# Kernel optimization log

Hardware: AMD Instinct MI355X
Metric: run time of the kernel (lower is better)

## Reference

```python
import jax, jax.numpy as jnp
import numpy as np

LN_EPS = 1e-5


def _ln(x, g, b):
    m = jnp.mean(x, axis=-1, keepdims=True)
    v = jnp.mean((x - m) ** 2, axis=-1, keepdims=True)
    return (x - m) * jax.lax.rsqrt(v + LN_EPS) * g + b


def _swish(x):
    return x * jax.nn.sigmoid(x)


def _ffn(x, w1, b1, w2, b2):
    return _swish(x @ w1 + b1) @ w2 + b2


def _dwconv(x, w, pad_l, pad_r):
    # x: (B,T,C), w: (C,K) depthwise kernel along time
    C = x.shape[-1]
    y = jax.lax.conv_general_dilated(
        jnp.transpose(x, (0, 2, 1)), w[:, None, :],
        window_strides=(1,), padding=[(pad_l, pad_r)],
        feature_group_count=C,
        dimension_numbers=('NCH', 'OIH', 'NCH'))
    return jnp.transpose(y, (0, 2, 1))


def _rel_shift(x):
    # NeMo Transformer-XL relative shift. x: (B,H,T,P)
    b, h, q, p = x.shape
    x = jnp.pad(x, ((0, 0), (0, 0), (0, 0), (1, 0)))
    x = x.reshape(b, h, p + 1, q)[:, :, 1:]
    return x.reshape(b, h, q, p)


def _mamba(x, in_proj_w, conv_w, conv_b, x_proj_w, dt_proj_w, dt_proj_b, A_log, D, out_proj_w):
    # Mamba1 selective-scan SSM. x: (B,T,d_model)
    B, T, _ = x.shape
    d_inner, d_state = A_log.shape
    dt_rank = dt_proj_w.shape[0]
    xi, z = jnp.split(x @ in_proj_w, 2, axis=-1)            # (B,T,d_inner) each
    K = conv_w.shape[1]
    xc = jax.nn.silu(_dwconv(xi, conv_w, K - 1, 0) + conv_b)  # causal depthwise conv
    dbc = xc @ x_proj_w
    dt = dbc[..., :dt_rank]
    Bs = dbc[..., dt_rank:dt_rank + d_state]                # (B,T,n)
    Cs = dbc[..., dt_rank + d_state:]                       # (B,T,n)
    dt = jax.nn.softplus(dt @ dt_proj_w + dt_proj_b)        # (B,T,d_inner)
    A = -jnp.exp(A_log)                                     # (d_inner,n)
    dA = jnp.exp(dt[..., None] * A)                         # (B,T,d,n)
    dBx = dt[..., None] * Bs[:, :, None, :] * xc[..., None]  # (B,T,d,n)

    def step(h, inp):
        dA_t, dBx_t, C_t = inp
        h = dA_t * h + dBx_t                                # (B,d,n)
        y = jnp.einsum('bdn,bn->bd', h, C_t)
        return h, y

    h0 = jnp.zeros((B, d_inner, d_state), x.dtype)
    _, ys = jax.lax.scan(step, h0, (jnp.moveaxis(dA, 1, 0), jnp.moveaxis(dBx, 1, 0), jnp.moveaxis(Cs, 1, 0)))
    y = jnp.moveaxis(ys, 0, 1) + D * xc
    y = y * jax.nn.silu(z)
    return y @ out_proj_w


def _rel_attn(x, pos_emb, wq, bq, wk, bk, wv, bv, w_pos, pbu, pbv, wo, bo):
    B, T, d = x.shape
    H = pbu.shape[0]
    dk = d // H
    q = (x @ wq + bq).reshape(B, T, H, dk)                  # (B,T,H,dk)
    k = (x @ wk + bk).reshape(B, T, H, dk).transpose(0, 2, 1, 3)
    v = (x @ wv + bv).reshape(B, T, H, dk).transpose(0, 2, 1, 3)
    p = (pos_emb @ w_pos).reshape(1, -1, H, dk).transpose(0, 2, 1, 3)  # (1,H,2T-1,dk)
    q_u = (q + pbu).transpose(0, 2, 1, 3)
    q_v = (q + pbv).transpose(0, 2, 1, 3)
    ac = jnp.einsum('bhqd,bhkd->bhqk', q_u, k)
    bd = jnp.einsum('bhqd,xhpd->bhqp', q_v, p)
    bd = _rel_shift(bd)[:, :, :, :T]
    scores = (ac + bd) / jnp.sqrt(jnp.asarray(dk, x.dtype))
    attn = jax.nn.softmax(scores, axis=-1)
    out = jnp.einsum('bhqk,bhkd->bhqd', attn, v).transpose(0, 2, 1, 3).reshape(B, T, d)
    return out @ wo + bo


def _conv_module(x, pw1_w, pw1_b, dw_w, dw_b, bn_g, bn_b, pw2_w, pw2_b):
    a = x @ pw1_w + pw1_b
    h, g = jnp.split(a, 2, axis=-1)
    y = h * jax.nn.sigmoid(g)                               # GLU
    K = dw_w.shape[1]
    y = _dwconv(y, dw_w, (K - 1) // 2, (K - 1) // 2) + dw_b
    # BatchNorm in eval mode with running stats (mean=0, var=1)
    y = y * jax.lax.rsqrt(jnp.asarray(1.0 + LN_EPS, x.dtype)) * bn_g + bn_b
    return _swish(y) @ pw2_w + pw2_b


def _forward(x, pos_emb,
             ln1_g, ln1_b, ff1_w1, ff1_b1, ff1_w2, ff1_b2,
             mamba_ln_g, mamba_ln_b, in_proj_w, mconv_w, mconv_b, x_proj_w,
             dt_proj_w, dt_proj_b, A_log, D, out_proj_w,
             mlp_ln_g, mlp_ln_b, mlp_fc1_w, mlp_fc1_b, mlp_fc2_w, mlp_fc2_b,
             att_ln_g, att_ln_b, wq, bq, wk, bk, wv, bv, w_pos, pos_bias_u, pos_bias_v, wo, bo,
             conv_ln_g, conv_ln_b, pw1_w, pw1_b, dw_w, dw_b, bn_g, bn_b, pw2_w, pw2_b,
             ln2_g, ln2_b, ff2_w1, ff2_b1, ff2_w2, ff2_b2,
             out_ln_g, out_ln_b):
    # FFN1 (half-step)
    r = x + 0.5 * _ffn(_ln(x, ln1_g, ln1_b), ff1_w1, ff1_b1, ff1_w2, ff1_b2)
    # Mamba SSM block (prenorm residual, fc_factor=1)
    r = r + _mamba(_ln(r, mamba_ln_g, mamba_ln_b), in_proj_w, mconv_w, mconv_b,
                   x_proj_w, dt_proj_w, dt_proj_b, A_log, D, out_proj_w)
    # Gated MLP sublayer of the SSM block
    h = _ln(r, mlp_ln_g, mlp_ln_b) @ mlp_fc1_w + mlp_fc1_b
    u, g = jnp.split(h, 2, axis=-1)
    r = r + (u * jax.nn.silu(g)) @ mlp_fc2_w + mlp_fc2_b
    # Rel-pos self attention
    r = r + _rel_attn(_ln(r, att_ln_g, att_ln_b), pos_emb, wq, bq, wk, bk, wv, bv,
                      w_pos, pos_bias_u, pos_bias_v, wo, bo)
    # Conformer conv module
    r = r + _conv_module(_ln(r, conv_ln_g, conv_ln_b), pw1_w, pw1_b, dw_w, dw_b,
                         bn_g, bn_b, pw2_w, pw2_b)
    # FFN2 (half-step)
    r = r + 0.5 * _ffn(_ln(r, ln2_g, ln2_b), ff2_w1, ff2_b1, ff2_w2, ff2_b2)
    return _ln(r, out_ln_g, out_ln_b)


def setup_inputs() -> dict:
    key = jax.random.key(0)
    B, T, d = 8, 1024, 512
    d_ff = 2048
    n_heads, dk = 8, 64
    expand, d_state, d_conv = 2, 16, 4
    d_inner = expand * d
    dt_rank = d // 16
    mlp_hidden = 2 * d
    K = 31
    ks = iter(jax.random.split(key, 40))

    def rn(shape, s=0.02):
        return jax.random.normal(next(ks), shape, jnp.float32) * s

    f32 = jnp.float32
    inp = dict(
        x=jax.random.normal(next(ks), (B, T, d), f32),
        pos_emb=jax.random.normal(next(ks), (1, 2 * T - 1, d), f32),
        ln1_g=jnp.ones((d,), f32), ln1_b=jnp.zeros((d,), f32),
        ff1_w1=rn((d, d_ff)), ff1_b1=jnp.zeros((d_ff,), f32),
        ff1_w2=rn((d_ff, d)), ff1_b2=jnp.zeros((d,), f32),
        mamba_ln_g=jnp.ones((d,), f32), mamba_ln_b=jnp.zeros((d,), f32),
        in_proj_w=rn((d, 2 * d_inner)),
        mconv_w=rn((d_inner, d_conv), 0.1), mconv_b=jnp.zeros((d_inner,), f32),
        x_proj_w=rn((d_inner, dt_rank + 2 * d_state)),
        dt_proj_w=rn((dt_rank, d_inner), 0.1),
        dt_proj_b=jnp.full((d_inner,), float(np.log(np.expm1(0.01))), f32),
        A_log=jnp.log(jnp.broadcast_to(jnp.arange(1, d_state + 1, dtype=f32), (d_inner, d_state)) + 0.0),
        D=jnp.ones((d_inner,), f32),
        out_proj_w=rn((d_inner, d)),
        mlp_ln_g=jnp.ones((d,), f32), mlp_ln_b=jnp.zeros((d,), f32),
        mlp_fc1_w=rn((d, 2 * mlp_hidden)), mlp_fc1_b=jnp.zeros((2 * mlp_hidden,), f32),
        mlp_fc2_w=rn((mlp_hidden, d)), mlp_fc2_b=jnp.zeros((d,), f32),
        att_ln_g=jnp.ones((d,), f32), att_ln_b=jnp.zeros((d,), f32),
        wq=rn((d, d)), bq=jnp.zeros((d,), f32),
        wk=rn((d, d)), bk=jnp.zeros((d,), f32),
        wv=rn((d, d)), bv=jnp.zeros((d,), f32),
        w_pos=rn((d, d)),
        pos_bias_u=rn((n_heads, dk)), pos_bias_v=rn((n_heads, dk)),
        wo=rn((d, d)), bo=jnp.zeros((d,), f32),
        conv_ln_g=jnp.ones((d,), f32), conv_ln_b=jnp.zeros((d,), f32),
        pw1_w=rn((d, 2 * d)), pw1_b=jnp.zeros((2 * d,), f32),
        dw_w=rn((d, K), 0.1), dw_b=jnp.zeros((d,), f32),
        bn_g=jnp.ones((d,), f32), bn_b=jnp.zeros((d,), f32),
        pw2_w=rn((d, d)), pw2_b=jnp.zeros((d,), f32),
        ln2_g=jnp.ones((d,), f32), ln2_b=jnp.zeros((d,), f32),
        ff2_w1=rn((d, d_ff)), ff2_b1=jnp.zeros((d_ff,), f32),
        ff2_w2=rn((d_ff, d)), ff2_b2=jnp.zeros((d,), f32),
        out_ln_g=jnp.ones((d,), f32), out_ln_b=jnp.zeros((d,), f32),
    )
    return inp


def reference(x, pos_emb,
              ln1_g, ln1_b, ff1_w1, ff1_b1, ff1_w2, ff1_b2,
              mamba_ln_g, mamba_ln_b, in_proj_w, mconv_w, mconv_b, x_proj_w,
              dt_proj_w, dt_proj_b, A_log, D, out_proj_w,
              mlp_ln_g, mlp_ln_b, mlp_fc1_w, mlp_fc1_b, mlp_fc2_w, mlp_fc2_b,
              att_ln_g, att_ln_b, wq, bq, wk, bk, wv, bv, w_pos, pos_bias_u, pos_bias_v, wo, bo,
              conv_ln_g, conv_ln_b, pw1_w, pw1_b, dw_w, dw_b, bn_g, bn_b, pw2_w, pw2_b,
              ln2_g, ln2_b, ff2_w1, ff2_b1, ff2_w2, ff2_b2,
              out_ln_g, out_ln_b):
    return _forward(x, pos_emb,
                    ln1_g, ln1_b, ff1_w1, ff1_b1, ff1_w2, ff1_b2,
                    mamba_ln_g, mamba_ln_b, in_proj_w, mconv_w, mconv_b, x_proj_w,
                    dt_proj_w, dt_proj_b, A_log, D, out_proj_w,
                    mlp_ln_g, mlp_ln_b, mlp_fc1_w, mlp_fc1_b, mlp_fc2_w, mlp_fc2_b,
                    att_ln_g, att_ln_b, wq, bq, wk, bk, wv, bv, w_pos, pos_bias_u, pos_bias_v, wo, bo,
                    conv_ln_g, conv_ln_b, pw1_w, pw1_b, dw_w, dw_b, bn_g, bn_b, pw2_w, pw2_b,
                    ln2_g, ln2_b, ff2_w1, ff2_b1, ff2_w2, ff2_b2,
                    out_ln_g, out_ln_b)
```

## Files before the change

### kernel.cpp

```cpp
#include <hip/hip_runtime.h>


typedef __bf16 bf16;
typedef __bf16 bf16x8 __attribute__((ext_vector_type(8)));
typedef __bf16 bf16x4 __attribute__((ext_vector_type(4)));
typedef float  f32x4  __attribute__((ext_vector_type(4)));

__device__ __forceinline__ float sigmf(float x) { return 1.f / (1.f + __expf(-x)); }
__device__ __forceinline__ float softplusf(float x) { return x > 20.f ? x : log1pf(__expf(x)); }

#define GL16(gsrc, ldst) \
  __builtin_amdgcn_global_load_lds((const __attribute__((address_space(1))) void*)(gsrc), \
                                   (__attribute__((address_space(3))) void*)(ldst), 16, 0, 0)

struct PrepEnt { const float* src; unsigned long long dstOff; int K, N, stride, mode, blk0, pad; };
#define NPREP 21
struct PrepTab { PrepEnt e[NPREP]; };

__global__ __launch_bounds__(256) void prep_weights(PrepTab tab, char* ws)
{
  int e = 0;
  for (int i = 1; i < NPREP; ++i) if ((int)blockIdx.x >= tab.e[i].blk0) e = i;
  PrepEnt en = tab.e[e];
  int lb = blockIdx.x - en.blk0;
  int tid = threadIdx.x;
  if (en.mode == 0) {
    __shared__ float t[32][33];
    int nTk = (en.K + 31) >> 5;
    int kt = lb % nTk, nt = lb / nTk;
    int k0 = kt * 32, n0 = nt * 32;
    int c = tid & 31, r0 = tid >> 5;
#pragma unroll
    for (int p = 0; p < 4; ++p) {
      int r = r0 + p * 8;
      int gk = k0 + r, gn = n0 + c;
      t[r][c] = (gk < en.K && gn < en.N) ? en.src[(size_t)gk * en.N + gn] : 0.f;
    }
    __syncthreads();
    bf16* dst = (bf16*)(ws + en.dstOff);
#pragma unroll
    for (int p = 0; p < 4; ++p) {
      int r = r0 + p * 8;
      int gn = n0 + r, gk = k0 + c;
      if (gn < en.N && gk < en.K) dst[(size_t)gn * en.stride + gk] = (bf16)t[c][r];
    }
  } else if (en.mode == 1) {
    size_t total = (size_t)en.K * en.N;
    size_t i0 = (size_t)lb * 2048 + (size_t)tid * 8;
    if (i0 < total) {
      bf16* dst = (bf16*)(ws + en.dstOff);
#pragma unroll
      for (int i = 0; i < 8; ++i) dst[i0 + i] = (bf16)en.src[i0 + i];
    }
  } else {
    int i0 = lb * 256 + tid;
    if (i0 < en.N) ((float*)(ws + en.dstOff))[i0] = en.src[i0];
  }
}

template<int MODE>
__global__ __launch_bounds__(256)
void gemm_k(const bf16* __restrict__ A, const bf16* __restrict__ W,
            const float* __restrict__ bias, const float* __restrict__ res,
            float* __restrict__ outF, bf16* __restrict__ outB,
            int M, int N, int K)
{
  __shared__ __align__(16) char As[128 * 128];
  __shared__ __align__(16) char Bs[128 * 128];
  const int tid = threadIdx.x;
  const int w = tid >> 6, l = tid & 63, l15 = l & 15, lg = l >> 4;
  const int wr = w >> 1, wc = w & 1;
  const int m0 = blockIdx.y * 128, n0 = blockIdx.x * 128;
  const int Mm1 = M - 1;
  f32x4 acc[4][4] = {};

  for (int k0 = 0; k0 < K; k0 += 64) {
#pragma unroll
    for (int i = 0; i < 4; ++i) {
      int row = w * 32 + i * 8 + (l >> 3);
      int ar = m0 + row; ar = ar > Mm1 ? Mm1 : ar;
      GL16(A + (size_t)ar * K + k0 + (l & 7) * 8, As + (w * 32 + i * 8) * 128);
      GL16(W + (size_t)(n0 + row) * K + k0 + (l & 7) * 8, Bs + (w * 32 + i * 8) * 128);
    }
    __syncthreads();
#pragma unroll
    for (int ks = 0; ks < 2; ++ks) {
      bf16x8 af[4], bfv[4];
#pragma unroll
      for (int mi = 0; mi < 4; ++mi)
        af[mi] = *(const bf16x8*)(As + (wr * 64 + mi * 16 + l15) * 128 + (ks * 4 + lg) * 16);
#pragma unroll
      for (int ni = 0; ni < 4; ++ni)
        bfv[ni] = *(const bf16x8*)(Bs + (wc * 64 + ni * 16 + l15) * 128 + (ks * 4 + lg) * 16);
#pragma unroll
      for (int mi = 0; mi < 4; ++mi)
#pragma unroll
        for (int ni = 0; ni < 4; ++ni)
          acc[mi][ni] = __builtin_amdgcn_mfma_f32_16x16x32_bf16(af[mi], bfv[ni], acc[mi][ni], 0, 0, 0);
    }
    __syncthreads();
  }

#pragma unroll
  for (int ni = 0; ni < 4; ++ni) {
    int col = n0 + wc * 64 + ni * 16 + l15;
    float bvl = 0.f;
    if constexpr (MODE == 2 || MODE == 3 || MODE == 4 || MODE == 5 || MODE == 7) bvl = bias[col];
#pragma unroll
    for (int mi = 0; mi < 4; ++mi) {
#pragma unroll
      for (int r = 0; r < 4; ++r) {
        int row = m0 + wr * 64 + mi * 16 + lg * 4 + r;
        if (row >= M) continue;
        float v = acc[mi][ni][r];
        size_t oi = (size_t)row * N + col;
        if constexpr (MODE == 0) { outF[oi] = v; }
        else if constexpr (MODE == 1) { outB[oi] = (bf16)v; }
        else if constexpr (MODE == 2) { outB[oi] = (bf16)(v + bvl); }
        else if constexpr (MODE == 3) { float t = v + bvl; outB[oi] = (bf16)(t * sigmf(t)); }
        else if constexpr (MODE == 4) { outF[oi] = res[oi] + v + bvl; }
        else if constexpr (MODE == 5) { outF[oi] = res[oi] + 0.5f * (v + bvl); }
        else if constexpr (MODE == 6) { outF[oi] = res[oi] + v; }
        else if constexpr (MODE == 7) { outF[oi] = softplusf(v + bvl); }
        else if constexpr (MODE == 8) {
          int hd = col >> 6;
          outB[((size_t)hd * 2047 + row) * 64 + (col & 63)] = (bf16)v;
        }
      }
    }
  }
}

template<bool F32OUT>
__global__ __launch_bounds__(128)
void ln_k(const float* __restrict__ in, const float* __restrict__ g,
          const float* __restrict__ bb, void* __restrict__ out)
{
  int row = blockIdx.x, t = threadIdx.x;
  float4 v = ((const float4*)(in + (size_t)row * 512))[t];
  float s  = v.x + v.y + v.z + v.w;
  float s2 = v.x * v.x + v.y * v.y + v.z * v.z + v.w * v.w;
#pragma unroll
  for (int o = 1; o < 64; o <<= 1) { s += __shfl_xor(s, o); s2 += __shfl_xor(s2, o); }
  __shared__ float sh[4];
  if ((t & 63) == 0) { sh[(t >> 6) * 2] = s; sh[(t >> 6) * 2 + 1] = s2; }
  __syncthreads();
  s = sh[0] + sh[2]; s2 = sh[1] + sh[3];
  float mean = s * (1.f / 512.f);
  float var  = s2 * (1.f / 512.f) - mean * mean;
  float rstd = rsqrtf(var + 1e-5f);
  float4 gg = ((const float4*)g)[t], bv = ((const float4*)bb)[t];
  float o0 = (v.x - mean) * rstd * gg.x + bv.x;
  float o1 = (v.y - mean) * rstd * gg.y + bv.y;
  float o2 = (v.z - mean) * rstd * gg.z + bv.z;
  float o3 = (v.w - mean) * rstd * gg.w + bv.w;
  if constexpr (F32OUT) {
    ((float4*)out)[(size_t)row * 128 + t] = make_float4(o0, o1, o2, o3);
  } else {
    bf16x4 ob; ob[0] = (bf16)o0; ob[1] = (bf16)o1; ob[2] = (bf16)o2; ob[3] = (bf16)o3;
    ((bf16x4*)out)[(size_t)row * 128 + t] = ob;
  }
}

template<int VAR>
__global__ __launch_bounds__(256)
void glu_k(const bf16* __restrict__ in, void* __restrict__ out,
           int halfN, int fullN, int shift)
{
  int gid = blockIdx.x * 256 + threadIdx.x;
  int m = gid >> shift;
  int j = (gid & ((1 << shift) - 1)) * 8;
  bf16x8 uv = *(const bf16x8*)(in + (size_t)m * fullN + j);
  bf16x8 gv = *(const bf16x8*)(in + (size_t)m * fullN + halfN + j);
  if constexpr (VAR == 0) {
    bf16x8 o;
#pragma unroll
    for (int i = 0; i < 8; ++i) {
      float gf = (float)gv[i];
      o[i] = (bf16)((float)uv[i] * gf * sigmf(gf));
    }
    *(bf16x8*)((bf16*)out + (size_t)m * halfN + j) = o;
  } else {
    float* of = (float*)out + (size_t)m * halfN + j;
    float4 a, b;
    a.x = (float)uv[0] * sigmf((float)gv[0]); a.y = (float)uv[1] * sigmf((float)gv[1]);
    a.z = (float)uv[2] * sigmf((float)gv[2]); a.w = (float)uv[3] * sigmf((float)gv[3]);
    b.x = (float)uv[4] * sigmf((float)gv[4]); b.y = (float)uv[5] * sigmf((float)gv[5]);
    b.z = (float)uv[6] * sigmf((float)gv[6]); b.w = (float)uv[7] * sigmf((float)gv[7]);
    *(float4*)of = a; *(float4*)(of + 4) = b;
  }
}

__global__ __launch_bounds__(256)
void extract_dt(const float* __restrict__ dbc, bf16* __restrict__ dtb)
{
  int gid = blockIdx.x * 256 + threadIdx.x;
  int m = gid >> 3, j = (gid & 7) * 8;
  bf16x8 o;
#pragma unroll
  for (int i = 0; i < 8; ++i) {
    int c = j + i;
    o[i] = (bf16)(c < 32 ? dbc[(size_t)m * 128 + c] : 0.f);
  }
  *(bf16x8*)(dtb + (size_t)m * 64 + j) = o;
}

__global__ __launch_bounds__(256)
void dwconv4_k(const bf16* __restrict__ xz, const float* __restrict__ cw,
               const float* __restrict__ cb, bf16* __restrict__ xcb)
{
  const int c  = blockIdx.x * 256 + threadIdx.x;
  const int t0 = blockIdx.y * 16;
  const int b  = blockIdx.z;
  const bf16* xb = xz + (size_t)b * 1024 * 2048 + c;
  float win[19];
#pragma unroll
  for (int j = 0; j < 19; ++j) {
    int tt = t0 - 3 + j;
    win[j] = (tt >= 0) ? (float)xb[(size_t)tt * 2048] : 0.f;
  }
  float w0 = cw[c * 4], w1 = cw[c * 4 + 1], w2 = cw[c * 4 + 2], w3 = cw[c * 4 + 3];
  float cbv = cb[c];
  bf16* ob = xcb + (size_t)(b * 1024 + t0) * 1024 + c;
#pragma unroll
  for (int i = 0; i < 16; ++i) {
    float acc = cbv + win[i] * w0 + win[i + 1] * w1 + win[i + 2] * w2 + win[i + 3] * w3;
    ob[(size_t)i * 1024] = (bf16)(acc * sigmf(acc));
  }
}

__global__ __launch_bounds__(256)
void dwconv31_k(const float* __restrict__ y, const float* __restrict__ dw,
                const float* __restrict__ db, const float* __restrict__ bg,
                const float* __restrict__ bb, bf16* __restrict__ outb)
{
  const int c  = blockIdx.x * 256 + threadIdx.x;
  const int t0 = blockIdx.y * 32;
  const int b  = blockIdx.z;
  const float* yb = y + (size_t)b * 1024 * 512 + c;
  float win[62];
#pragma unroll
  for (int j = 0; j < 62; ++j) {
    int tt = t0 - 15 + j;
    win[j] = (tt >= 0 && tt < 1024) ? yb[(size_t)tt * 512] : 0.f;
  }
  float wt[31];
#pragma unroll
  for (int k = 0; k < 31; ++k) wt[k] = dw[c * 31 + k];
  const float bgv = bg[c] * rsqrtf(1.f + 1e-5f);
  const float bbv = bb[c], dbv = db[c];
  bf16* ob = outb + (size_t)(b * 1024 + t0) * 512 + c;
#pragma unroll
  for (int i = 0; i < 32; ++i) {
    float acc = dbv;
#pragma unroll
    for (int k = 0; k < 31; ++k) acc += win[i + k] * wt[k];
    float v = acc * bgv + bbv;
    ob[(size_t)i * 512] = (bf16)(v * sigmf(v));
  }
}

__global__ __launch_bounds__(128)
void scan_k(const float* __restrict__ dt, const bf16* __restrict__ xc,
            const bf16* __restrict__ xz, const float* __restrict__ dbc,
            const float* __restrict__ alog, const float* __restrict__ Dp,
            bf16* __restrict__ ym)
{
  __shared__ __align__(16) float dtb[2][64][32];
  __shared__ __align__(16) bf16  xcb[2][64][32];
  __shared__ __align__(16) bf16  zbb[2][64][32];
  __shared__ __align__(16) float bcb[2][64][32];
  __shared__ __align__(16) float yp[64][128];
  __shared__ float Ds[32];

  const int tid = threadIdx.x;
  const int w = tid >> 6, l = tid & 63;
  const int ch = tid >> 2;
  const int s  = tid & 3;
  const int b  = blockIdx.x >> 5, dc = blockIdx.x & 31;
  const int d0 = dc * 32;
  const int d  = d0 + ch;

  const float A0 = -__expf(alog[d * 16 + s * 4 + 0]);
  const float A1 = -__expf(alog[d * 16 + s * 4 + 1]);
  const float A2 = -__expf(alog[d * 16 + s * 4 + 2]);
  const float A3 = -__expf(alog[d * 16 + s * 4 + 3]);
  if (tid < 32) Ds[tid] = Dp[d0 + tid];
  float h0 = 0.f, h1 = 0.f, h2 = 0.f, h3 = 0.f;
  const size_t rb = (size_t)b * 1024;

  auto stage = [&](int bu, int c) {
    size_t t0 = rb + (size_t)c * 64;
#pragma unroll
    for (int i = 0; i < 4; ++i) {
      int r = w * 32 + i * 8 + (l >> 3);
      GL16(dt + (t0 + r) * 1024 + d0 + (l & 7) * 4, &dtb[bu][w * 32 + i * 8][0]);
    }
#pragma unroll
    for (int i = 0; i < 4; ++i) {
      int r = w * 32 + i * 8 + (l >> 3);
      GL16(dbc + (t0 + r) * 128 + 32 + (l & 7) * 4, &bcb[bu][w * 32 + i * 8][0]);
    }
#pragma unroll
    for (int i = 0; i < 2; ++i) {
      int r = w * 32 + i * 16 + (l >> 2);
      GL16(xc + (t0 + r) * 1024 + d0 + (l & 3) * 8, &xcb[bu][w * 32 + i * 16][0]);
      GL16(xz + (t0 + r) * 2048 + 1024 + d0 + (l & 3) * 8, &zbb[bu][w * 32 + i * 16][0]);
    }
  };

  stage(0, 0);
  __syncthreads();
  int bu = 0;
  for (int c = 0; c < 16; ++c) {
    if (c < 15) stage(bu ^ 1, c + 1);
#pragma unroll 8
    for (int t = 0; t < 64; ++t) {
      float dtv = dtb[bu][t][ch];
      float xcv = (float)xcb[bu][t][ch];
      float4 Bv = *(const float4*)&bcb[bu][t][s * 4];
      float4 Cv = *(const float4*)&bcb[bu][t][16 + s * 4];
      float dtx = dtv * xcv;
      h0 = __expf(dtv * A0) * h0 + dtx * Bv.x;
      h1 = __expf(dtv * A1) * h1 + dtx * Bv.y;
      h2 = __expf(dtv * A2) * h2 + dtx * Bv.z;
      h3 = __expf(dtv * A3) * h3 + dtx * Bv.w;
      yp[t][tid] = h0 * Cv.x + h1 * Cv.y + h2 * Cv.z + h3 * Cv.w;
    }
    __syncthreads();
    {
      size_t t0 = rb + (size_t)c * 64;
#pragma unroll
      for (int j = 0; j < 16; ++j) {
        int idx = j * 128 + tid;
        int t = idx >> 5, cc = idx & 31;
        float4 p = *(const float4*)&yp[t][cc * 4];
        float xcv = (float)xcb[bu][t][cc];
        float zv  = (float)zbb[bu][t][cc];
        float o = (p.x + p.y + p.z + p.w + Ds[cc] * xcv) * (zv * sigmf(zv));
        ym[(t0 + t) * 1024 + d0 + cc] = (bf16)o;
      }
    }
    __syncthreads();
    bu ^= 1;
  }
}

__global__ __launch_bounds__(256)
void attnprep_k(const bf16* __restrict__ qkv, const float* __restrict__ pbu,
                const float* __restrict__ pbv, bf16* __restrict__ qu,
                bf16* __restrict__ qv, bf16* __restrict__ kb)
{
  int gid = blockIdx.x * 256 + threadIdx.x;
  int dd = (gid & 7) * 8;
  int t  = (gid >> 3) & 1023;
  int h  = (gid >> 13) & 7;
  int b  = gid >> 16;
  size_t src = ((size_t)(b * 1024 + t)) * 1536 + h * 64 + dd;
  bf16x8 q = *(const bf16x8*)(qkv + src);
  bf16x8 k = *(const bf16x8*)(qkv + src + 512);
  size_t dst = (((size_t)(b * 8 + h)) * 1024 + t) * 64 + dd;
  bf16x8 ou, ov;
#pragma unroll
  for (int i = 0; i < 8; ++i) {
    float qf = (float)q[i];
    ou[i] = (bf16)(qf + pbu[h * 64 + dd + i]);
    ov[i] = (bf16)(qf + pbv[h * 64 + dd + i]);
  }
  *(bf16x8*)(qu + dst) = ou;
  *(bf16x8*)(qv + dst) = ov;
  *(bf16x8*)(kb + dst) = k;
}

__global__ __launch_bounds__(256)
void vtrans_k(const bf16* __restrict__ qkv, bf16* __restrict__ vt)
{
  __shared__ __align__(16) bf16 tile[64][80];
  int tid = threadIdx.x;
  int t0 = blockIdx.x * 64, h = blockIdx.y, b = blockIdx.z;
#pragma unroll
  for (int j = 0; j < 2; ++j) {
    int idx = tid + j * 256;
    int r = idx >> 3, c8 = (idx & 7) * 8;
    bf16x8 v = *(const bf16x8*)(qkv + ((size_t)(b * 1024 + t0 + r)) * 1536 + 1024 + h * 64 + c8);
    *(bf16x8*)(&tile[r][c8]) = v;
  }
  __syncthreads();
  size_t obase = ((size_t)(b * 8 + h)) * 64;
#pragma unroll
  for (int j = 0; j < 2; ++j) {
    int idx = tid + j * 256;
    int ddr = idx >> 3, tc = (idx & 7) * 8;
    bf16x8 o;
#pragma unroll
    for (int i = 0; i < 8; ++i) o[i] = tile[tc + i][ddr];
    *(bf16x8*)(vt + (obase + ddr) * 1024 + t0 + tc) = o;
  }
}

__global__ __launch_bounds__(256)
void attn_k(const bf16* __restrict__ qu, const bf16* __restrict__ qv,
            const bf16* __restrict__ kb, const bf16* __restrict__ vt,
            const bf16* __restrict__ ph, bf16* __restrict__ outb)
{
  __shared__ __align__(16) char Ks[64 * 128];
  __shared__ __align__(16) char Vs[64 * 128];
  __shared__ __align__(16) bf16 Pl[4][16][88];
  int tid = threadIdx.x, w = tid >> 6, l = tid & 63;
  int l15 = l & 15, lg = l >> 4;
  int qt = blockIdx.x, h = blockIdx.y, b = blockIdx.z;
  int bh = b * 8 + h;
  int qw0 = qt * 64 + w * 16;
  const bf16* kbh = kb + (size_t)bh * 65536;
  const bf16* vth = vt + (size_t)bh * 65536;
  const bf16* phh = ph + (size_t)h * 2047 * 64;

  bf16x8 aqu[2], aqv[2], onesf;
#pragma unroll
  for (int i = 0; i < 8; ++i) onesf[i] = (bf16)1.f;
  {
    size_t qb = ((size_t)bh * 1024 + qw0 + l15) * 64 + lg * 8;
    aqu[0] = *(const bf16x8*)(qu + qb);
    aqu[1] = *(const bf16x8*)(qu + qb + 32);
    aqv[0] = *(const bf16x8*)(qv + qb);
    aqv[1] = *(const bf16x8*)(qv + qb + 32);
  }
  f32x4 acco[4] = {};
  f32x4 accl = {};

  for (int kv = 0; kv < 16; ++kv) {
    int k0 = kv * 64;
#pragma unroll
    for (int j = 0; j < 2; ++j) {
      int idx = tid + j * 256;
      int row = idx >> 3, sl = idx & 7, ssl = sl ^ (row & 7);
      *(bf16x8*)(Ks + row * 128 + ssl * 16) = *(const bf16x8*)(kbh + (size_t)(k0 + row) * 64 + sl * 8);
      *(bf16x8*)(Vs + row * 128 + ssl * 16) = *(const bf16x8*)(vth + (size_t)row * 1024 + k0 + sl * 8);
    }
    __syncthreads();
    f32x4 sfr[4] = {};
    f32x4 efr[5] = {};
#pragma unroll
    for (int ni = 0; ni < 4; ++ni)
#pragma unroll
      for (int kt = 0; kt < 2; ++kt) {
        int row = ni * 16 + l15;
        int ssl = (kt * 4 + lg) ^ (row & 7);
        bf16x8 bv = *(const bf16x8*)(Ks + row * 128 + ssl * 16);
        sfr[ni] = __builtin_amdgcn_mfma_f32_16x16x32_bf16(aqu[kt], bv, sfr[ni], 0, 0, 0);
      }
    int rho0 = k0 - qw0 + 1008;
#pragma unroll
    for (int f = 0; f < 5; ++f) {
      int rho = rho0 + f * 16 + l15; if (rho > 2046) rho = 2046;
      const bf16* pp = phh + (size_t)rho * 64;
#pragma unroll
      for (int kt = 0; kt < 2; ++kt) {
        bf16x8 bv = *(const bf16x8*)(pp + kt * 32 + lg * 8);
        efr[f] = __builtin_amdgcn_mfma_f32_16x16x32_bf16(aqv[kt], bv, efr[f], 0, 0, 0);
      }
    }
#pragma unroll
    for (int r = 0; r < 4; ++r) {
      int qr = lg * 4 + r;
#pragma unroll
      for (int ni = 0; ni < 4; ++ni) {
        int j = ni * 16 + l15 - qr + 15;
        int srcl = (l & 48) | (j & 15);
        float v1 = __shfl(efr[ni][r], srcl, 64);
        float v2 = __shfl(efr[ni + 1][r], srcl, 64);
        float bd = ((j >> 4) == ni) ? v1 : v2;
        Pl[w][qr][ni * 16 + l15] = (bf16)__expf((sfr[ni][r] + bd) * 0.125f);
      }
    }
#pragma unroll
    for (int kt = 0; kt < 2; ++kt) {
      bf16x8 af = *(const bf16x8*)(&Pl[w][l15][kt * 32 + lg * 8]);
      accl = __builtin_amdgcn_mfma_f32_16x16x32_bf16(af, onesf, accl, 0, 0, 0);
#pragma unroll
      for (int ni = 0; ni < 4; ++ni) {
        int row = ni * 16 + l15;
        int ssl = (kt * 4 + lg) ^ (row & 7);
        bf16x8 bv = *(const bf16x8*)(Vs + row * 128 + ssl * 16);
        acco[ni] = __builtin_amdgcn_mfma_f32_16x16x32_bf16(af, bv, acco[ni], 0, 0, 0);
      }
    }
    __syncthreads();
  }
#pragma unroll
  for (int r = 0; r < 4; ++r) {
    float inv = 1.f / accl[r];
    int grow = b * 1024 + qw0 + lg * 4 + r;
#pragma unroll
    for (int ni = 0; ni < 4; ++ni)
      outb[(size_t)grow * 512 + h * 64 + ni * 16 + l15] = (bf16)(acco[ni][r] * inv);
  }
}

extern "C" void kernel_launch(void* const* d_in, const int* in_sizes, int n_in,
                              void* d_out, int out_size, void* d_ws, size_t ws_size,
                              hipStream_t stream)
{
  char* ws = (char*)d_ws;
  const float* x        = (const float*)d_in[0];
  const float* pos_emb  = (const float*)d_in[1];
  const float* ln1_g    = (const float*)d_in[2];
  const float* ln1_b    = (const float*)d_in[3];
  const float* ff1_w1   = (const float*)d_in[4];
  const float* ff1_b1   = (const float*)d_in[5];
  const float* ff1_w2   = (const float*)d_in[6];
  const float* ff1_b2   = (const float*)d_in[7];
  const float* mamba_ln_g = (const float*)d_in[8];
  const float* mamba_ln_b = (const float*)d_in[9];
  const float* in_proj_w  = (const float*)d_in[10];
  const float* mconv_w    = (const float*)d_in[11];
  const float* mconv_b    = (const float*)d_in[12];
  const float* x_proj_w   = (const float*)d_in[13];
  const float* dt_proj_w  = (const float*)d_in[14];
  const float* dt_proj_b  = (const float*)d_in[15];
  const float* A_log      = (const float*)d_in[16];
  const float* Dvec       = (const float*)d_in[17];
  const float* out_proj_w = (const float*)d_in[18];
  const float* mlp_ln_g   = (const float*)d_in[19];
  const float* mlp_ln_b   = (const float*)d_in[20];
  const float* mlp_fc1_w  = (const float*)d_in[21];
  const float* mlp_fc1_b  = (const float*)d_in[22];
  const float* mlp_fc2_w  = (const float*)d_in[23];
  const float* mlp_fc2_b  = (const float*)d_in[24];
  const float* att_ln_g   = (const float*)d_in[25];
  const float* att_ln_b   = (const float*)d_in[26];
  const float* wq  = (const float*)d_in[27];
  const float* bq  = (const float*)d_in[28];
  const float* wk  = (const float*)d_in[29];
  const float* bk  = (const float*)d_in[30];
  const float* wv  = (const float*)d_in[31];
  const float* bvv = (const float*)d_in[32];
  const float* w_pos = (const float*)d_in[33];
  const float* pbu   = (const float*)d_in[34];
  const float* pbv   = (const float*)d_in[35];
  const float* wo  = (const float*)d_in[36];
  const float* bo  = (const float*)d_in[37];
  const float* conv_ln_g = (const float*)d_in[38];
  const float* conv_ln_b = (const float*)d_in[39];
  const float* pw1_w = (const float*)d_in[40];
  const float* pw1_b = (const float*)d_in[41];
  const float* dw_w  = (const float*)d_in[42];
  const float* dw_b  = (const float*)d_in[43];
  const float* bn_g  = (const float*)d_in[44];
  const float* bn_b  = (const float*)d_in[45];
  const float* pw2_w = (const float*)d_in[46];
  const float* pw2_b = (const float*)d_in[47];
  const float* ln2_g = (const float*)d_in[48];
  const float* ln2_b = (const float*)d_in[49];
  const float* ff2_w1 = (const float*)d_in[50];
  const float* ff2_b1 = (const float*)d_in[51];
  const float* ff2_w2 = (const float*)d_in[52];
  const float* ff2_b2 = (const float*)d_in[53];
  const float* out_ln_g = (const float*)d_in[54];
  const float* out_ln_b = (const float*)d_in[55];

  size_t off = 0;
  auto alloc = [&](size_t bytes) { size_t r = off; off += (bytes + 255) & ~(size_t)255; return r; };
  const size_t o_ff1w1t  = alloc((size_t)2048 * 512 * 2);
  const size_t o_ff1w2t  = alloc((size_t)512 * 2048 * 2);
  const size_t o_inprojt = alloc((size_t)2048 * 512 * 2);
  const size_t o_xprojt  = alloc((size_t)128 * 1024 * 2);
  const size_t o_dtprojt = alloc((size_t)1024 * 64 * 2);
  const size_t o_outprojt= alloc((size_t)512 * 1024 * 2);
  const size_t o_fc1t    = alloc((size_t)2048 * 512 * 2);
  const size_t o_fc2t    = alloc((size_t)512 * 1024 * 2);
  const size_t o_wqkvt   = alloc((size_t)1536 * 512 * 2);
  const size_t o_wpost   = alloc((size_t)512 * 512 * 2);
  const size_t o_wot     = alloc((size_t)512 * 512 * 2);
  const size_t o_pw1t    = alloc((size_t)1024 * 512 * 2);
  const size_t o_pw2t    = alloc((size_t)512 * 512 * 2);
  const size_t o_ff2w1t  = alloc((size_t)2048 * 512 * 2);
  const size_t o_ff2w2t  = alloc((size_t)512 * 2048 * 2);
  const size_t o_posbf   = alloc((size_t)2047 * 512 * 2);
  const size_t o_pheads  = alloc((size_t)8 * 2047 * 64 * 2);
  const size_t o_bqkv    = alloc((size_t)1536 * 4);
  const size_t o_R       = alloc((size_t)8192 * 512 * 4);
  const size_t o_ABUF    = alloc((size_t)8192 * 512 * 2);
  const size_t o_GBUF    = alloc((size_t)8192 * 1024 * 2);
  const size_t o_DBC     = alloc((size_t)8192 * 128 * 4);
  const size_t o_DTBF    = alloc((size_t)8192 * 64 * 2);
  const size_t o_ARENA   = alloc((size_t)64 << 20);

  if (off > ws_size) return;

  bf16* ff1w1t  = (bf16*)(ws + o_ff1w1t);
  bf16* ff1w2t  = (bf16*)(ws + o_ff1w2t);
  bf16* inprojt = (bf16*)(ws + o_inprojt);
  bf16* xprojt  = (bf16*)(ws + o_xprojt);
  bf16* dtprojt = (bf16*)(ws + o_dtprojt);
  bf16* outprojt= (bf16*)(ws + o_outprojt);
  bf16* fc1t    = (bf16*)(ws + o_fc1t);
  bf16* fc2t    = (bf16*)(ws + o_fc2t);
  bf16* wqkvt   = (bf16*)(ws + o_wqkvt);
  bf16* wpost   = (bf16*)(ws + o_wpost);
  bf16* wot     = (bf16*)(ws + o_wot);
  bf16* pw1t    = (bf16*)(ws + o_pw1t);
  bf16* pw2t    = (bf16*)(ws + o_pw2t);
  bf16* ff2w1t  = (bf16*)(ws + o_ff2w1t);
  bf16* ff2w2t  = (bf16*)(ws + o_ff2w2t);
  bf16* posbf   = (bf16*)(ws + o_posbf);
  bf16* pheads  = (bf16*)(ws + o_pheads);
  float* bqkv   = (float*)(ws + o_bqkv);
  float* R      = (float*)(ws + o_R);
  bf16* ABUF    = (bf16*)(ws + o_ABUF);
  bf16* GBUF    = (bf16*)(ws + o_GBUF);
  float* GBUFf  = (float*)(ws + o_GBUF);
  float* DBC    = (float*)(ws + o_DBC);
  bf16* DTBF    = (bf16*)(ws + o_DTBF);
  char* ARENA   = ws + o_ARENA;
  bf16* BIGBF   = (bf16*)ARENA;
  bf16* XZB     = (bf16*)ARENA;
  float* DTF    = (float*)(ARENA + ((size_t)32 << 20));
  bf16* QKV     = (bf16*)ARENA;
  bf16* QU      = (bf16*)(ARENA + ((size_t)32 << 20));
  bf16* QV      = (bf16*)(ARENA + ((size_t)40 << 20));
  bf16* KB      = (bf16*)(ARENA + ((size_t)48 << 20));
  bf16* VT      = (bf16*)(ARENA + ((size_t)56 << 20));
  bf16* CBUF    = (bf16*)ARENA;
  float* OUT = (float*)d_out;

  (void)hipMemsetAsync(ws + o_xprojt, 0, (size_t)128 * 1024 * 2, stream);
  (void)hipMemsetAsync(ws + o_dtprojt, 0, (size_t)1024 * 64 * 2, stream);

  PrepTab tab;
  int nb = 0, ei = 0;
  auto addT = [&](const float* s, size_t dst, int K, int N, int stride) {
    int blks = ((K + 31) / 32) * ((N + 31) / 32);
    tab.e[ei] = { s, (unsigned long long)dst, K, N, stride, 0, nb, 0 };
    nb += blks; ++ei;
  };
  auto addC16 = [&](const float* s, size_t dst, int total) {
    int blks = (total + 2047) / 2048;
    tab.e[ei] = { s, (unsigned long long)dst, total, 1, 0, 1, nb, 0 };
    nb += blks; ++ei;
  };
  auto addC32 = [&](const float* s, size_t dst, int n) {
    int blks = (n + 255) / 256;
    tab.e[ei] = { s, (unsigned long long)dst, 1, n, 0, 2, nb, 0 };
    nb += blks; ++ei;
  };
  addT(ff1_w1,   o_ff1w1t,  512, 2048, 512);
  addT(ff1_w2,   o_ff1w2t,  2048, 512, 2048);
  addT(in_proj_w,o_inprojt, 512, 2048, 512);
  addT(x_proj_w, o_xprojt,  1024, 64, 1024);
  addT(dt_proj_w,o_dtprojt, 32, 1024, 64);
  addT(out_proj_w,o_outprojt,1024, 512, 1024);
  addT(mlp_fc1_w,o_fc1t,    512, 2048, 512);
  addT(mlp_fc2_w,o_fc2t,    1024, 512, 1024);
  addT(wq,       o_wqkvt,                         512, 512, 512);
  addT(wk,       o_wqkvt + (size_t)512 * 512 * 2, 512, 512, 512);
  addT(wv,       o_wqkvt + (size_t)1024 * 512 * 2,512, 512, 512);
  addT(w_pos,    o_wpost,   512, 512, 512);
  addT(wo,       o_wot,     512, 512, 512);
  addT(pw1_w,    o_pw1t,    512, 1024, 512);
  addT(pw2_w,    o_pw2t,    512, 512, 512);
  addT(ff2_w1,   o_ff2w1t,  512, 2048, 512);
  addT(ff2_w2,   o_ff2w2t,  2048, 512, 2048);
  addC16(pos_emb, o_posbf, 2047 * 512);
  addC32(bq, o_bqkv,            512);
  addC32(bk, o_bqkv + 512 * 4,  512);
  addC32(bvv,o_bqkv + 1024 * 4, 512);
  prep_weights<<<nb, 256, 0, stream>>>(tab, ws);

  gemm_k<8><<<dim3(4, 16), 256, 0, stream>>>(posbf, wpost, nullptr, nullptr, nullptr, pheads, 2047, 512, 512);

  ln_k<false><<<8192, 128, 0, stream>>>(x, ln1_g, ln1_b, ABUF);
  gemm_k<3><<<dim3(16, 64), 256, 0, stream>>>(ABUF, ff1w1t, ff1_b1, nullptr, nullptr, BIGBF, 8192, 2048, 512);
  gemm_k<5><<<dim3(4, 64), 256, 0, stream>>>(BIGBF, ff1w2t, ff1_b2, x, R, nullptr, 8192, 512, 2048);

  ln_k<false><<<8192, 128, 0, stream>>>(R, mamba_ln_g, mamba_ln_b, ABUF);
  gemm_k<1><<<dim3(16, 64), 256, 0, stream>>>(ABUF, inprojt, nullptr, nullptr, nullptr, XZB, 8192, 2048, 512);
  dwconv4_k<<<dim3(4, 64, 8), 256, 0, stream>>>(XZB, mconv_w, mconv_b, GBUF);
  gemm_k<0><<<dim3(1, 64), 256, 0, stream>>>(GBUF, xprojt, nullptr, nullptr, DBC, nullptr, 8192, 128, 1024);
  extract_dt<<<256, 256, 0, stream>>>(DBC, DTBF);
  gemm_k<7><<<dim3(8, 64), 256, 0, stream>>>(DTBF, dtprojt, dt_proj_b, nullptr, DTF, nullptr, 8192, 1024, 64);
  scan_k<<<256, 128, 0, stream>>>(DTF, GBUF, XZB, DBC, A_log, Dvec, GBUF);
  gemm_k<6><<<dim3(4, 64), 256, 0, stream>>>(GBUF, outprojt, nullptr, R, R, nullptr, 8192, 512, 1024);

  ln_k<false><<<8192, 128, 0, stream>>>(R, mlp_ln_g, mlp_ln_b, ABUF);
  gemm_k<2><<<dim3(16, 64), 256, 0, stream>>>(ABUF, fc1t, mlp_fc1_b, nullptr, nullptr, BIGBF, 8192, 2048, 512);
  glu_k<0><<<4096, 256, 0, stream>>>(BIGBF, GBUF, 1024, 2048, 7);
  gemm_k<4><<<dim3(4, 64), 256, 0, stream>>>(GBUF, fc2t, mlp_fc2_b, R, R, nullptr, 8192, 512, 1024);

  ln_k<false><<<8192, 128, 0, stream>>>(R, att_ln_g, att_ln_b, ABUF);
  gemm_k<2><<<dim3(12, 64), 256, 0, stream>>>(ABUF, wqkvt, bqkv, nullptr, nullptr, QKV, 8192, 1536, 512);
  attnprep_k<<<2048, 256, 0, stream>>>(QKV, pbu, pbv, QU, QV, KB);
  vtrans_k<<<dim3(16, 8, 8), 256, 0, stream>>>(QKV, VT);
  attn_k<<<dim3(16, 8, 8), 256, 0, stream>>>(QU, QV, KB, VT, pheads, ABUF);
  gemm_k<4><<<dim3(4, 64), 256, 0, stream>>>(ABUF, wot, bo, R, R, nullptr, 8192, 512, 512);

  ln_k<false><<<8192, 128, 0, stream>>>(R, conv_ln_g, conv_ln_b, ABUF);
  gemm_k<2><<<dim3(8, 64), 256, 0, stream>>>(ABUF, pw1t, pw1_b, nullptr, nullptr, CBUF, 8192, 1024, 512);
  glu_k<1><<<2048, 256, 0, stream>>>(CBUF, GBUFf, 512, 1024, 6);
  dwconv31_k<<<dim3(2, 32, 8), 256, 0, stream>>>(GBUFf, dw_w, dw_b, bn_g, bn_b, ABUF);
  gemm_k<4><<<dim3(4, 64), 256, 0, stream>>>(ABUF, pw2t, pw2_b, R, R, nullptr, 8192, 512, 512);

  ln_k<false><<<8192, 128, 0, stream>>>(R, ln2_g, ln2_b, ABUF);
  gemm_k<3><<<dim3(16, 64), 256, 0, stream>>>(ABUF, ff2w1t, ff2_b1, nullptr, nullptr, BIGBF, 8192, 2048, 512);
  gemm_k<5><<<dim3(4, 64), 256, 0, stream>>>(BIGBF, ff2w2t, ff2_b2, R, R, nullptr, 8192, 512, 2048);

  ln_k<true><<<8192, 128, 0, stream>>>(R, out_ln_g, out_ln_b, OUT);
}
```

Measured before the change: 1.088 ms.

## Split Mamba selective scan into chunked two-pass parallel scan

Replaces the single sequential scan kernel, which walked all 1024 timesteps per block, with a two-pass chunked scan. The first pass computes each 64-step chunk's local end state and the sum of dt from a zero start. The second pass rebuilds the incoming state from the earlier chunks' summaries, then re-runs its chunk and writes the gated output. This exposes far more parallel blocks than the 256 blocks of 128 threads used before. In exchange it recomputes the recurrence twice, adds workspace for chunk summaries, and loads straight from global memory instead of using LDS staging.

```diff
diff --git a/kernel.cpp b/kernel.cpp
--- a/kernel.cpp
+++ b/kernel.cpp
@@ -260,89 +260,86 @@
   }
 }
 
-__global__ __launch_bounds__(128)
-void scan_k(const float* __restrict__ dt, const bf16* __restrict__ xc,
-            const bf16* __restrict__ xz, const float* __restrict__ dbc,
-            const float* __restrict__ alog, const float* __restrict__ Dp,
-            bf16* __restrict__ ym)
-{
-  __shared__ __align__(16) float dtb[2][64][32];
-  __shared__ __align__(16) bf16  xcb[2][64][32];
-  __shared__ __align__(16) bf16  zbb[2][64][32];
-  __shared__ __align__(16) float bcb[2][64][32];
-  __shared__ __align__(16) float yp[64][128];
-  __shared__ float Ds[32];
-
+__global__ __launch_bounds__(256)
+void scan1_k(const float* __restrict__ dt, const bf16* __restrict__ xc,
+             const float* __restrict__ dbc, const float* __restrict__ alog,
+             float* __restrict__ QC, float* __restrict__ SC)
+{
   const int tid = threadIdx.x;
-  const int w = tid >> 6, l = tid & 63;
-  const int ch = tid >> 2;
-  const int s  = tid & 3;
-  const int b  = blockIdx.x >> 5, dc = blockIdx.x & 31;
-  const int d0 = dc * 32;
-  const int d  = d0 + ch;
-
+  const int ch = tid >> 2, s = tid & 3;
+  const int d = blockIdx.x * 64 + ch;
+  const int c = blockIdx.y, b = blockIdx.z;
   const float A0 = -__expf(alog[d * 16 + s * 4 + 0]);
   const float A1 = -__expf(alog[d * 16 + s * 4 + 1]);
   const float A2 = -__expf(alog[d * 16 + s * 4 + 2]);
   const float A3 = -__expf(alog[d * 16 + s * 4 + 3]);
-  if (tid < 32) Ds[tid] = Dp[d0 + tid];
+  float h0 = 0.f, h1 = 0.f, h2 = 0.f, h3 = 0.f, Sacc = 0.f;
+  const size_t r0 = (size_t)b * 1024 + c * 64;
+#pragma unroll 4
+  for (int t = 0; t < 64; ++t) {
+    size_t row = r0 + t;
+    float dtv = dt[row * 1024 + d];
+    float xcv = (float)xc[row * 1024 + d];
+    float4 Bv = *(const float4*)(dbc + row * 128 + 32 + s * 4);
+    float dtx = dtv * xcv;
+    Sacc += dtv;
+    h0 = __expf(dtv * A0) * h0 + dtx * Bv.x;
+    h1 = __expf(dtv * A1) * h1 + dtx * Bv.y;
+    h2 = __expf(dtv * A2) * h2 + dtx * Bv.z;
+    h3 = __expf(dtv * A3) * h3 + dtx * Bv.w;
+  }
+  size_t qi = (((size_t)(b * 16 + c)) * 1024 + d) * 16 + s * 4;
+  *(float4*)(QC + qi) = make_float4(h0, h1, h2, h3);
+  if (s == 0) SC[((size_t)(b * 16 + c)) * 1024 + d] = Sacc;
+}
+
+__global__ __launch_bounds__(256)
+void scan2_k(const float* __restrict__ dt, const bf16* __restrict__ xc,
+             const bf16* __restrict__ xz, const float* __restrict__ dbc,
+             const float* __restrict__ alog, const float* __restrict__ Dp,
+             const float* __restrict__ QC, const float* __restrict__ SC,
+             bf16* __restrict__ ym)
+{
+  const int tid = threadIdx.x;
+  const int ch = tid >> 2, s = tid & 3;
+  const int d = blockIdx.x * 64 + ch;
+  const int c = blockIdx.y, b = blockIdx.z;
+  const float A0 = -__expf(alog[d * 16 + s * 4 + 0]);
+  const float A1 = -__expf(alog[d * 16 + s * 4 + 1]);
+  const float A2 = -__expf(alog[d * 16 + s * 4 + 2]);
+  const float A3 = -__expf(alog[d * 16 + s * 4 + 3]);
+  const float Dv = Dp[d];
   float h0 = 0.f, h1 = 0.f, h2 = 0.f, h3 = 0.f;
-  const size_t rb = (size_t)b * 1024;
-
-  auto stage = [&](int bu, int c) {
-    size_t t0 = rb + (size_t)c * 64;
-#pragma unroll
-    for (int i = 0; i < 4; ++i) {
-      int r = w * 32 + i * 8 + (l >> 3);
-      GL16(dt + (t0 + r) * 1024 + d0 + (l & 7) * 4, &dtb[bu][w * 32 + i * 8][0]);
-    }
-#pragma unroll
-    for (int i = 0; i < 4; ++i) {
-      int r = w * 32 + i * 8 + (l >> 3);
-      GL16(dbc + (t0 + r) * 128 + 32 + (l & 7) * 4, &bcb[bu][w * 32 + i * 8][0]);
-    }
-#pragma unroll
-    for (int i = 0; i < 2; ++i) {
-      int r = w * 32 + i * 16 + (l >> 2);
-      GL16(xc + (t0 + r) * 1024 + d0 + (l & 3) * 8, &xcb[bu][w * 32 + i * 16][0]);
-      GL16(xz + (t0 + r) * 2048 + 1024 + d0 + (l & 3) * 8, &zbb[bu][w * 32 + i * 16][0]);
-    }
-  };
-
-  stage(0, 0);
-  __syncthreads();
-  int bu = 0;
-  for (int c = 0; c < 16; ++c) {
-    if (c < 15) stage(bu ^ 1, c + 1);
-#pragma unroll 8
-    for (int t = 0; t < 64; ++t) {
-      float dtv = dtb[bu][t][ch];
-      float xcv = (float)xcb[bu][t][ch];
-      float4 Bv = *(const float4*)&bcb[bu][t][s * 4];
-      float4 Cv = *(const float4*)&bcb[bu][t][16 + s * 4];
-      float dtx = dtv * xcv;
-      h0 = __expf(dtv * A0) * h0 + dtx * Bv.x;
-      h1 = __expf(dtv * A1) * h1 + dtx * Bv.y;
-      h2 = __expf(dtv * A2) * h2 + dtx * Bv.z;
-      h3 = __expf(dtv * A3) * h3 + dtx * Bv.w;
-      yp[t][tid] = h0 * Cv.x + h1 * Cv.y + h2 * Cv.z + h3 * Cv.w;
-    }
-    __syncthreads();
-    {
-      size_t t0 = rb + (size_t)c * 64;
-#pragma unroll
-      for (int j = 0; j < 16; ++j) {
-        int idx = j * 128 + tid;
-        int t = idx >> 5, cc = idx & 31;
-        float4 p = *(const float4*)&yp[t][cc * 4];
-        float xcv = (float)xcb[bu][t][cc];
-        float zv  = (float)zbb[bu][t][cc];
-        float o = (p.x + p.y + p.z + p.w + Ds[cc] * xcv) * (zv * sigmf(zv));
-        ym[(t0 + t) * 1024 + d0 + cc] = (bf16)o;
-      }
-    }
-    __syncthreads();
-    bu ^= 1;
+  for (int cp = 0; cp < c; ++cp) {
+    size_t ci = ((size_t)(b * 16 + cp)) * 1024 + d;
+    float S = SC[ci];
+    float4 q = *(const float4*)(QC + ci * 16 + s * 4);
+    h0 = __expf(S * A0) * h0 + q.x;
+    h1 = __expf(S * A1) * h1 + q.y;
+    h2 = __expf(S * A2) * h2 + q.z;
+    h3 = __expf(S * A3) * h3 + q.w;
+  }
+  const size_t r0 = (size_t)b * 1024 + c * 64;
+#pragma unroll 4
+  for (int t = 0; t < 64; ++t) {
+    size_t row = r0 + t;
+    float dtv = dt[row * 1024 + d];
+    float xcv = (float)xc[row * 1024 + d];
+    float zv  = (float)xz[row * 2048 + 1024 + d];
+    float4 Bv = *(const float4*)(dbc + row * 128 + 32 + s * 4);
+    float4 Cv = *(const float4*)(dbc + row * 128 + 48 + s * 4);
+    float dtx = dtv * xcv;
+    h0 = __expf(dtv * A0) * h0 + dtx * Bv.x;
+    h1 = __expf(dtv * A1) * h1 + dtx * Bv.y;
+    h2 = __expf(dtv * A2) * h2 + dtx * Bv.z;
+    h3 = __expf(dtv * A3) * h3 + dtx * Bv.w;
+    float yv = h0 * Cv.x + h1 * Cv.y + h2 * Cv.z + h3 * Cv.w;
+    yv += __shfl_xor(yv, 1);
+    yv += __shfl_xor(yv, 2);
+    if (s == 0) {
+      float o = (yv + Dv * xcv) * (zv * sigmf(zv));
+      ym[row * 1024 + d] = (bf16)o;
+    }
   }
 }
 
@@ -584,6 +581,8 @@
   const size_t o_GBUF    = alloc((size_t)8192 * 1024 * 2);
   const size_t o_DBC     = alloc((size_t)8192 * 128 * 4);
   const size_t o_DTBF    = alloc((size_t)8192 * 64 * 2);
+  const size_t o_QC      = alloc((size_t)8 * 16 * 1024 * 16 * 4);
+  const size_t o_SC      = alloc((size_t)8 * 16 * 1024 * 4);
   const size_t o_ARENA   = alloc((size_t)64 << 20);
 
   if (off > ws_size) return;
@@ -612,6 +611,8 @@
   float* GBUFf  = (float*)(ws + o_GBUF);
   float* DBC    = (float*)(ws + o_DBC);
   bf16* DTBF    = (bf16*)(ws + o_DTBF);
+  float* QC     = (float*)(ws + o_QC);
+  float* SC     = (float*)(ws + o_SC);
   char* ARENA   = ws + o_ARENA;
   bf16* BIGBF   = (bf16*)ARENA;
   bf16* XZB     = (bf16*)ARENA;
@@ -679,7 +680,8 @@
   gemm_k<0><<<dim3(1, 64), 256, 0, stream>>>(GBUF, xprojt, nullptr, nullptr, DBC, nullptr, 8192, 128, 1024);
   extract_dt<<<256, 256, 0, stream>>>(DBC, DTBF);
   gemm_k<7><<<dim3(8, 64), 256, 0, stream>>>(DTBF, dtprojt, dt_proj_b, nullptr, DTF, nullptr, 8192, 1024, 64);
-  scan_k<<<256, 128, 0, stream>>>(DTF, GBUF, XZB, DBC, A_log, Dvec, GBUF);
+  scan1_k<<<dim3(16, 16, 8), 256, 0, stream>>>(DTF, GBUF, DBC, A_log, QC, SC);
+  scan2_k<<<dim3(16, 16, 8), 256, 0, stream>>>(DTF, GBUF, XZB, DBC, A_log, Dvec, QC, SC, GBUF);
   gemm_k<6><<<dim3(4, 64), 256, 0, stream>>>(GBUF, outprojt, nullptr, R, R, nullptr, 8192, 512, 1024);
 
   ln_k<false><<<8192, 128, 0, stream>>>(R, mlp_ln_g, mlp_ln_b, ABUF);
```

Result: slower. 1.282 ms (+17.9%).

## Fuse dt projection GEMM and softplus into the selective scan kernel

Applied to the files above, without the earlier changes.

Removes the separate dt_proj GEMM that wrote a full fp32 dt tensor (B*T x d_inner) to global memory. The scan kernel now loads the low-rank bf16 dt slice per chunk plus its slice of the projection weights, and computes dt with a small MFMA GEMM followed by softplus into shared memory. That GEMM for the next chunk is placed after the current chunk's output stage. This saves a kernel launch and a large fp32 write and read, but adds work and shared memory to the scan, which may lower its occupancy and lengthen its serial critical path.

```diff
diff --git a/kernel.cpp b/kernel.cpp
--- a/kernel.cpp
+++ b/kernel.cpp
@@ -105,7 +105,7 @@
   for (int ni = 0; ni < 4; ++ni) {
     int col = n0 + wc * 64 + ni * 16 + l15;
     float bvl = 0.f;
-    if constexpr (MODE == 2 || MODE == 3 || MODE == 4 || MODE == 5 || MODE == 7) bvl = bias[col];
+    if constexpr (MODE == 2 || MODE == 3 || MODE == 4 || MODE == 5) bvl = bias[col];
 #pragma unroll
     for (int mi = 0; mi < 4; ++mi) {
 #pragma unroll
@@ -121,7 +121,6 @@
         else if constexpr (MODE == 4) { outF[oi] = res[oi] + v + bvl; }
         else if constexpr (MODE == 5) { outF[oi] = res[oi] + 0.5f * (v + bvl); }
         else if constexpr (MODE == 6) { outF[oi] = res[oi] + v; }
-        else if constexpr (MODE == 7) { outF[oi] = softplusf(v + bvl); }
         else if constexpr (MODE == 8) {
           int hd = col >> 6;
           outB[((size_t)hd * 2047 + row) * 64 + (col & 63)] = (bf16)v;
@@ -261,20 +260,25 @@
 }
 
 __global__ __launch_bounds__(128)
-void scan_k(const float* __restrict__ dt, const bf16* __restrict__ xc,
+void scan_k(const bf16* __restrict__ dtbf, const bf16* __restrict__ wp,
+            const float* __restrict__ dtbias, const bf16* __restrict__ xc,
             const bf16* __restrict__ xz, const float* __restrict__ dbc,
             const float* __restrict__ alog, const float* __restrict__ Dp,
             bf16* __restrict__ ym)
 {
-  __shared__ __align__(16) float dtb[2][64][32];
+  __shared__ __align__(16) bf16  dtbfb[2][64][64];
+  __shared__ __align__(16) bf16  wproj[32][64];
+  __shared__ __align__(16) float dtb[64][32];
   __shared__ __align__(16) bf16  xcb[2][64][32];
   __shared__ __align__(16) bf16  zbb[2][64][32];
   __shared__ __align__(16) float bcb[2][64][32];
   __shared__ __align__(16) float yp[64][128];
   __shared__ float Ds[32];
+  __shared__ float biass[32];
 
   const int tid = threadIdx.x;
   const int w = tid >> 6, l = tid & 63;
+  const int l15 = l & 15, lg = l >> 4;
   const int ch = tid >> 2;
   const int s  = tid & 3;
   const int b  = blockIdx.x >> 5, dc = blockIdx.x & 31;
@@ -285,7 +289,7 @@
   const float A1 = -__expf(alog[d * 16 + s * 4 + 1]);
   const float A2 = -__expf(alog[d * 16 + s * 4 + 2]);
   const float A3 = -__expf(alog[d * 16 + s * 4 + 3]);
-  if (tid < 32) Ds[tid] = Dp[d0 + tid];
+  if (tid < 32) { Ds[tid] = Dp[d0 + tid]; biass[tid] = dtbias[d0 + tid]; }
   float h0 = 0.f, h1 = 0.f, h2 = 0.f, h3 = 0.f;
   const size_t rb = (size_t)b * 1024;
 
@@ -294,7 +298,7 @@
 #pragma unroll
     for (int i = 0; i < 4; ++i) {
       int r = w * 32 + i * 8 + (l >> 3);
-      GL16(dt + (t0 + r) * 1024 + d0 + (l & 7) * 4, &dtb[bu][w * 32 + i * 8][0]);
+      GL16(dtbf + (t0 + r) * 64 + (l & 7) * 8, &dtbfb[bu][w * 32 + i * 8][0]);
     }
 #pragma unroll
     for (int i = 0; i < 4; ++i) {
@@ -309,14 +313,51 @@
     }
   };
 
+  auto minigemm = [&](int sb) {
+    f32x4 dacc[2][2] = {};
+#pragma unroll
+    for (int ks = 0; ks < 2; ++ks) {
+      bf16x8 af[2], bfv[2];
+#pragma unroll
+      for (int mi = 0; mi < 2; ++mi)
+        af[mi] = *(const bf16x8*)&dtbfb[sb][w * 32 + mi * 16 + l15][ks * 32 + lg * 8];
+#pragma unroll
+      for (int ni = 0; ni < 2; ++ni)
+        bfv[ni] = *(const bf16x8*)&wproj[ni * 16 + l15][ks * 32 + lg * 8];
+#pragma unroll
+      for (int mi = 0; mi < 2; ++mi)
+#pragma unroll
+        for (int ni = 0; ni < 2; ++ni)
+          dacc[mi][ni] = __builtin_amdgcn_mfma_f32_16x16x32_bf16(af[mi], bfv[ni], dacc[mi][ni], 0, 0, 0);
+    }
+#pragma unroll
+    for (int mi = 0; mi < 2; ++mi)
+#pragma unroll
+      for (int ni = 0; ni < 2; ++ni)
+#pragma unroll
+        for (int r = 0; r < 4; ++r) {
+          int t = w * 32 + mi * 16 + lg * 4 + r;
+          int dd = ni * 16 + l15;
+          dtb[t][dd] = softplusf(dacc[mi][ni][r] + biass[dd]);
+        }
+  };
+
+#pragma unroll
+  for (int i = 0; i < 2; ++i) {
+    int r = w * 16 + i * 8 + (l >> 3);
+    GL16(wp + (size_t)(d0 + r) * 64 + (l & 7) * 8, &wproj[w * 16 + i * 8][0]);
+  }
   stage(0, 0);
   __syncthreads();
+  minigemm(0);
+  __syncthreads();
+
   int bu = 0;
   for (int c = 0; c < 16; ++c) {
     if (c < 15) stage(bu ^ 1, c + 1);
 #pragma unroll 8
     for (int t = 0; t < 64; ++t) {
-      float dtv = dtb[bu][t][ch];
+      float dtv = dtb[t][ch];
       float xcv = (float)xcb[bu][t][ch];
       float4 Bv = *(const float4*)&bcb[bu][t][s * 4];
       float4 Cv = *(const float4*)&bcb[bu][t][16 + s * 4];
@@ -341,6 +382,7 @@
         ym[(t0 + t) * 1024 + d0 + cc] = (bf16)o;
       }
     }
+    if (c < 15) minigemm(bu ^ 1);
     __syncthreads();
     bu ^= 1;
   }
@@ -615,7 +657,6 @@
   char* ARENA   = ws + o_ARENA;
   bf16* BIGBF   = (bf16*)ARENA;
   bf16* XZB     = (bf16*)ARENA;
-  float* DTF    = (float*)(ARENA + ((size_t)32 << 20));
   bf16* QKV     = (bf16*)ARENA;
   bf16* QU      = (bf16*)(ARENA + ((size_t)32 << 20));
   bf16* QV      = (bf16*)(ARENA + ((size_t)40 << 20));
@@ -678,8 +719,7 @@
   dwconv4_k<<<dim3(4, 64, 8), 256, 0, stream>>>(XZB, mconv_w, mconv_b, GBUF);
   gemm_k<0><<<dim3(1, 64), 256, 0, stream>>>(GBUF, xprojt, nullptr, nullptr, DBC, nullptr, 8192, 128, 1024);
   extract_dt<<<256, 256, 0, stream>>>(DBC, DTBF);
-  gemm_k<7><<<dim3(8, 64), 256, 0, stream>>>(DTBF, dtprojt, dt_proj_b, nullptr, DTF, nullptr, 8192, 1024, 64);
-  scan_k<<<256, 128, 0, stream>>>(DTF, GBUF, XZB, DBC, A_log, Dvec, GBUF);
+  scan_k<<<256, 128, 0, stream>>>(DTBF, dtprojt, dt_proj_b, GBUF, XZB, DBC, A_log, Dvec, GBUF);
   gemm_k<6><<<dim3(4, 64), 256, 0, stream>>>(GBUF, outprojt, nullptr, R, R, nullptr, 8192, 512, 1024);
 
   ln_k<false><<<8192, 128, 0, stream>>>(R, mlp_ln_g, mlp_ln_b, ABUF);
```

Measured after the change: 1.122 ms. +3.1%, slower.
